# Kernel tuning notes

Measured on AMD Instinct MI355X. Metric: run time of the kernel, lower is better.

The kernel has to match this reference:

```python
import jax, jax.numpy as jnp
import numpy as np

N = 65536      # nodes in batched graph
E = 2097152    # edges (avg degree 32)
V = 1000       # chord vocabulary size
F_IN = 128     # chord feature dim
H = 256        # hidden_dim
OUT = 128      # out_dim
G = 256        # number of graphs in batch


def _gcn_layer(x, W, b, row, col, norm, n):
    # x: [n, f_in] -> [n, f_out]; PyG GCNConv: linear then normalized aggregation + bias
    x = x @ W
    msg = x[row] * norm[:, None]            # gather at source, scale by sym-norm
    return jax.ops.segment_sum(msg, col, num_segments=n) + b


def setup_inputs() -> dict:
    key = jax.random.key(0)
    ks = jax.random.split(key, 9)
    chord_feats = jax.random.normal(ks[0], (V, F_IN), jnp.float32)
    W1 = jax.random.normal(ks[1], (F_IN, H), jnp.float32) * 0.05
    b1 = jnp.zeros((H,), jnp.float32)
    W2 = jax.random.normal(ks[2], (H, OUT), jnp.float32) * 0.05
    b2 = jnp.zeros((OUT,), jnp.float32)
    edge_attr = jax.random.uniform(ks[3], (E,), jnp.float32)          # positive edge weights
    node_indices = jax.random.randint(ks[4], (N,), 0, V, jnp.int64)
    edge_index = jax.random.randint(ks[5], (2, E), 0, N, jnp.int64)
    batch_index = jnp.sort(jax.random.randint(ks[6], (N,), 0, G, jnp.int64))
    return {"chord_feats": chord_feats, "W1": W1, "b1": b1, "W2": W2, "b2": b2,
            "edge_attr": edge_attr, "node_indices": node_indices,
            "edge_index": edge_index, "batch_index": batch_index}


def reference(chord_feats, W1, b1, W2, b2, edge_attr, node_indices, edge_index, batch_index):
    loops = jnp.arange(N, dtype=edge_index.dtype)
    row = jnp.concatenate([edge_index[0], loops])   # source
    col = jnp.concatenate([edge_index[1], loops])   # target
    ew = jnp.concatenate([edge_attr, jnp.ones((N,), edge_attr.dtype)])  # self-loop weight 1
    # symmetric GCN normalization: D^-1/2 A D^-1/2
    deg = jax.ops.segment_sum(ew, col, num_segments=N)
    dis = jnp.where(deg > 0, jax.lax.rsqrt(jnp.maximum(deg, 1e-30)), 0.0)
    norm = dis[row] * ew * dis[col]

    x = chord_feats[node_indices]                   # [N, F_IN]
    x = jax.nn.relu(_gcn_layer(x, W1, b1, row, col, norm, N))
    x = jax.nn.relu(_gcn_layer(x, W2, b2, row, col, norm, N))

    # global_mean_pool over batch_index
    sums = jax.ops.segment_sum(x, batch_index, num_segments=G)
    counts = jax.ops.segment_sum(jnp.ones((N,), x.dtype), batch_index, num_segments=G)
    return sums / jnp.maximum(counts, 1.0)[:, None]
```

## Files before the change

### kernel.cpp

```cpp
#include <hip/hip_runtime.h>
#include <hip/hip_fp16.h>
#include <math.h>

constexpr int N_NODES = 65536;
constexpr int N_EDGES = 2097152;
constexpr int F_IN    = 128;
constexpr int H_DIM   = 256;
constexpr int O_DIM   = 128;
constexpr int N_GRAPH = 256;
constexpr int V_SIZE  = 1000;

constexpr int EPB  = 8192;
constexpr int NBLK = N_EDGES / EPB;
constexpr float FXP = 16777216.0f;


__global__ void k_init(float* __restrict__ pool, const int* __restrict__ batch,
                       float* __restrict__ cntf, const float* __restrict__ cf,
                       const float* __restrict__ W1, __half* __restrict__ cfW1) {
    __shared__ float xs[8 * F_IN];
    int i = blockIdx.x * blockDim.x + threadIdx.x;
    if (i < N_GRAPH * O_DIM) pool[i] = 0.0f;
    if (blockIdx.x == 0) {
        int g = threadIdx.x;
        int lo = 0, hi = N_NODES;
        while (lo < hi) { int m = (lo + hi) >> 1; if (batch[m] < g) lo = m + 1; else hi = m; }
        int start = lo;
        lo = 0; hi = N_NODES;
        while (lo < hi) { int m = (lo + hi) >> 1; if (batch[m] <= g) lo = m + 1; else hi = m; }
        cntf[g] = (float)(lo - start);
    }
    if (blockIdx.x < V_SIZE / 8) {
        int rb = blockIdx.x * 8;
        int t  = threadIdx.x;
        #pragma unroll
        for (int p = 0; p < 4; ++p) {
            int idx = p * 256 + t;
            int r = idx >> 7, k = idx & 127;
            xs[idx] = cf[(size_t)(rb + r) * F_IN + k];
        }
        __syncthreads();
        float acc[8] = {};
        for (int k = 0; k < F_IN; ++k) {
            float w = W1[k * H_DIM + t];
            #pragma unroll
            for (int j = 0; j < 8; ++j) acc[j] += xs[j * F_IN + k] * w;
        }
        #pragma unroll
        for (int j = 0; j < 8; ++j)
            cfW1[(size_t)(rb + j) * H_DIM + t] = __float2half(acc[j]);
    }
}


__global__ void k_hist(const int* __restrict__ col, int* __restrict__ hist) {
    __shared__ int h[256];
    int t = threadIdx.x;
    h[t] = 0;
    __syncthreads();
    int base = blockIdx.x * EPB;
    #pragma unroll
    for (int i = 0; i < EPB / 256; ++i)
        atomicAdd(&h[col[base + i * 256 + t] >> 8], 1);
    __syncthreads();
    hist[t * NBLK + blockIdx.x] = h[t];
}


__global__ void k_scan1(const int* __restrict__ in, int* __restrict__ out,
                        int* __restrict__ bsum) {
    __shared__ int s[256];
    int tid = threadIdx.x;
    int i = blockIdx.x * 256 + tid;
    int v = in[i];
    s[tid] = v;
    __syncthreads();
    for (int d = 1; d < 256; d <<= 1) {
        int t = (tid >= d) ? s[tid - d] : 0;
        __syncthreads();
        s[tid] += t;
        __syncthreads();
    }
    out[i] = s[tid] - v;
    if (tid == 255) bsum[blockIdx.x] = s[255];
}

__global__ void k_scan2(int* __restrict__ bsum) {
    __shared__ int s[256];
    int tid = threadIdx.x;
    int v = bsum[tid];
    s[tid] = v;
    __syncthreads();
    for (int d = 1; d < 256; d <<= 1) {
        int t = (tid >= d) ? s[tid - d] : 0;
        __syncthreads();
        s[tid] += t;
        __syncthreads();
    }
    bsum[tid] = s[tid] - v;
}


__global__ void k_part(const int* __restrict__ row, const int* __restrict__ col,
                       const float* __restrict__ ew, const int* __restrict__ nidx,
                       const int* __restrict__ hoffs, const int* __restrict__ bsum,
                       int2* __restrict__ part) {
    __shared__ int cur[256];
    int t = threadIdx.x;
    cur[t] = hoffs[t * NBLK + blockIdx.x] + bsum[t];
    __syncthreads();
    int base = blockIdx.x * EPB;
    for (int i = 0; i < EPB / 256; ++i) {
        int e = base + i * 256 + t;
        int r = row[e], c = col[e];
        unsigned hw = (unsigned)__half_as_ushort(__float2half(ew[e]));
        int vb = nidx[r];
        int slot = atomicAdd(&cur[c >> 8], 1);
        int2 rec;
        rec.x = (r << 16) | ((c & 255) << 8) | (vb >> 2);
        rec.y = (int)(((unsigned)(vb & 3) << 16) | hw);
        part[slot] = rec;
    }
}


__global__ void k_build1(const int* __restrict__ hoffs, const int* __restrict__ bsum,
                         const int2* __restrict__ part, float* __restrict__ dis,
                         int* __restrict__ offs) {
    __shared__ unsigned long long dc[256];
    __shared__ int sc[256];
    int t = threadIdx.x;
    int bucket = blockIdx.x;
    dc[t] = 0ULL;
    __syncthreads();
    int start = hoffs[bucket * NBLK] + bsum[bucket];
    int end   = (bucket == 255) ? N_EDGES : (hoffs[(bucket + 1) * NBLK] + bsum[bucket + 1]);
    for (int j = start + t; j < end; j += 256) {
        int2 rec = part[j];
        int dst = (rec.x >> 8) & 255;
        float w = __half2float(__ushort_as_half((unsigned short)(rec.y & 0xFFFF)));
        atomicAdd(&dc[dst], (1ULL << 40) |
                  (unsigned long long)(unsigned)(w * FXP + 0.5f));
    }
    __syncthreads();
    unsigned long long v = dc[t];
    float deg = 1.0f + (float)(v & 0xFFFFFFFFFFULL) * (1.0f / FXP);
    dis[bucket * 256 + t] = 1.0f / sqrtf(deg);
    int cnt = (int)(v >> 40);
    sc[t] = cnt;
    __syncthreads();
    for (int d = 1; d < 256; d <<= 1) {
        int x = (t >= d) ? sc[t - d] : 0;
        __syncthreads();
        sc[t] += x;
        __syncthreads();
    }
    offs[bucket * 256 + t] = start + sc[t] - cnt;
    if (bucket == 255 && t == 255) offs[N_NODES] = N_EDGES;
}


__global__ void k_build2(const int* __restrict__ hoffs, const int* __restrict__ bsum,
                         const int2* __restrict__ part, const float* __restrict__ dis,
                         const int* __restrict__ offs, int2* __restrict__ csr) {
    __shared__ int cur[256];
    int t = threadIdx.x;
    int bucket = blockIdx.x;
    cur[t] = offs[bucket * 256 + t];
    __syncthreads();
    int start = hoffs[bucket * NBLK] + bsum[bucket];
    int end   = (bucket == 255) ? N_EDGES : (hoffs[(bucket + 1) * NBLK] + bsum[bucket + 1]);
    for (int j = start + t; j < end; j += 256) {
        int2 rec = part[j];
        int dst = (rec.x >> 8) & 255;
        unsigned src = ((unsigned)rec.x) >> 16;
        int vb = ((rec.x & 255) << 2) | ((rec.y >> 16) & 3);
        float w = __half2float(__ushort_as_half((unsigned short)(rec.y & 0xFFFF)));
        float nm = dis[src] * w;
        int slot = atomicAdd(&cur[dst], 1);
        int2 e;
        e.x = (int)((src << 10) | (unsigned)vb);
        e.y = __float_as_int(nm);
        csr[slot] = e;
    }
}


__global__ void k_agg1(const int2* __restrict__ cfW1, const int* __restrict__ nidx,
                       const float* __restrict__ dis, const int* __restrict__ offs,
                       const int2* __restrict__ csr, const float4* __restrict__ b1f4,
                       int2* __restrict__ h1) {
    int wave = threadIdx.x >> 6;
    int lane = threadIdx.x & 63;
    int c = blockIdx.x * 4 + wave;
    float d = dis[c];
    int2 sp = cfW1[(size_t)nidx[c] * 64 + lane];
    float2 sa = __half22float2(*(__half2*)&sp.x);
    float2 sb = __half22float2(*(__half2*)&sp.y);
    float4 esum = {0.f, 0.f, 0.f, 0.f};
    int a0 = offs[c], a1 = offs[c + 1];
    int s = a0;
    for (; s + 8 <= a1; s += 8) {
        int sb_i = __builtin_amdgcn_readfirstlane(s);
        int2 e[8];
        #pragma unroll
        for (int u = 0; u < 8; ++u) e[u] = csr[sb_i + u];
        int2 v[8];
        #pragma unroll
        for (int u = 0; u < 8; ++u)
            v[u] = cfW1[(size_t)(e[u].x & 1023) * 64 + lane];
        #pragma unroll
        for (int u = 0; u < 8; ++u) {
            float n = __int_as_float(e[u].y);
            float2 va = __half22float2(*(__half2*)&v[u].x);
            float2 vb = __half22float2(*(__half2*)&v[u].y);
            esum.x += va.x * n; esum.y += va.y * n;
            esum.z += vb.x * n; esum.w += vb.y * n;
        }
    }
    for (; s < a1; ++s) {
        int sb_i = __builtin_amdgcn_readfirstlane(s);
        int2 e0 = csr[sb_i];
        int2 v0 = cfW1[(size_t)(e0.x & 1023) * 64 + lane];
        float n = __int_as_float(e0.y);
        float2 va = __half22float2(*(__half2*)&v0.x);
        float2 vb = __half22float2(*(__half2*)&v0.y);
        esum.x += va.x * n; esum.y += va.y * n;
        esum.z += vb.x * n; esum.w += vb.y * n;
    }
    float4 bb = b1f4[lane];
    float dd = d * d;
    float r0 = bb.x + sa.x * dd + d * esum.x;
    float r1 = bb.y + sa.y * dd + d * esum.y;
    float r2 = bb.z + sb.x * dd + d * esum.z;
    float r3 = bb.w + sb.y * dd + d * esum.w;
    r0 = r0 > 0.f ? r0 : 0.f;  r1 = r1 > 0.f ? r1 : 0.f;
    r2 = r2 > 0.f ? r2 : 0.f;  r3 = r3 > 0.f ? r3 : 0.f;
    float2 p0 = {r0, r1}, p1 = {r2, r3};
    __half2 ha = __float22half2_rn(p0);
    __half2 hb = __float22half2_rn(p1);
    int2 outv;
    outv.x = *(int*)&ha;
    outv.y = *(int*)&hb;
    h1[(size_t)c * 64 + lane] = outv;
}


__global__ void k_gemm2(const __half* __restrict__ h1, const float* __restrict__ W2,
                        __half* __restrict__ xw2h) {
    __shared__ float xs[32 * H_DIM];
    int nb = blockIdx.x * 32;
    int t  = threadIdx.x;
    const int4* src = (const int4*)(h1 + (size_t)nb * H_DIM);
    float4* dst4 = (float4*)xs;
    #pragma unroll
    for (int p = 0; p < 4; ++p) {
        int4 pk = src[p * 256 + t];
        __half2 ha = *(__half2*)&pk.x, hb = *(__half2*)&pk.y;
        __half2 hc = *(__half2*)&pk.z, hd = *(__half2*)&pk.w;
        float2 fa = __half22float2(ha), fb = __half22float2(hb);
        float2 fc = __half22float2(hc), fd = __half22float2(hd);
        float4 A; A.x = fa.x; A.y = fa.y; A.z = fb.x; A.w = fb.y;
        float4 B; B.x = fc.x; B.y = fc.y; B.z = fd.x; B.w = fd.y;
        dst4[(p * 256 + t) * 2]     = A;
        dst4[(p * 256 + t) * 2 + 1] = B;
    }
    __syncthreads();
    int o  = t & 63;
    int jg = t >> 6;
    const float* xsj = xs + jg * 8 * H_DIM;
    float acc[8][2] = {};
    for (int k = 0; k < H_DIM; ++k) {
        float w0 = W2[k * O_DIM + o];
        float w1 = W2[k * O_DIM + o + 64];
        #pragma unroll
        for (int j = 0; j < 8; ++j) {
            float x = xsj[j * H_DIM + k];
            acc[j][0] += x * w0; acc[j][1] += x * w1;
        }
    }
    #pragma unroll
    for (int j = 0; j < 8; ++j) {
        size_t base = (size_t)(nb + jg * 8 + j) * O_DIM + o;
        xw2h[base]      = __float2half(acc[j][0]);
        xw2h[base + 64] = __float2half(acc[j][1]);
    }
}


__global__ void k_agg2_pool(const __half2* __restrict__ xw2h, const float* __restrict__ b2,
                            const float* __restrict__ dis, const int* __restrict__ offs,
                            const int2* __restrict__ csr, const int* __restrict__ batch,
                            float* __restrict__ pool) {
    __shared__ float2 red[4][64];
    __shared__ int bgs[4];
    int wave = threadIdx.x >> 6;
    int lane = threadIdx.x & 63;
    int c = blockIdx.x * 4 + wave;
    float d = dis[c];
    float2 self = __half22float2(xw2h[(size_t)c * 64 + lane]);
    float2 bb = ((const float2*)b2)[lane];
    float2 esum = {0.f, 0.f};
    int s0 = offs[c], s1 = offs[c + 1];
    int s = s0;
    for (; s + 8 <= s1; s += 8) {
        int sb_i = __builtin_amdgcn_readfirstlane(s);
        int2 e[8];
        #pragma unroll
        for (int u = 0; u < 8; ++u) e[u] = csr[sb_i + u];
        float2 v[8];
        #pragma unroll
        for (int u = 0; u < 8; ++u)
            v[u] = __half22float2(xw2h[(size_t)(e[u].x >> 10) * 64 + lane]);
        #pragma unroll
        for (int u = 0; u < 8; ++u) {
            float n = __int_as_float(e[u].y);
            esum.x += v[u].x * n; esum.y += v[u].y * n;
        }
    }
    for (; s < s1; ++s) {
        int sb_i = __builtin_amdgcn_readfirstlane(s);
        int2 e0 = csr[sb_i];
        float2 v0 = __half22float2(xw2h[(size_t)(e0.x >> 10) * 64 + lane]);
        float n0 = __int_as_float(e0.y);
        esum.x += v0.x * n0; esum.y += v0.y * n0;
    }
    float dd = d * d;
    float2 acc;
    acc.x = bb.x + self.x * dd + d * esum.x;
    acc.y = bb.y + self.y * dd + d * esum.y;
    acc.x = acc.x > 0.0f ? acc.x : 0.0f;
    acc.y = acc.y > 0.0f ? acc.y : 0.0f;
    red[wave][lane] = acc;
    if (lane == 0) bgs[wave] = batch[c];
    __syncthreads();
    if (wave == 0) {
        float2 a = red[0][lane];
        int cg = bgs[0];
        #pragma unroll
        for (int w = 1; w < 4; ++w) {
            int g = bgs[w];
            float2 r = red[w][lane];
            if (g == cg) { a.x += r.x; a.y += r.y; }
            else {
                atomicAdd(&pool[cg * O_DIM + 2 * lane], a.x);
                atomicAdd(&pool[cg * O_DIM + 2 * lane + 1], a.y);
                a = r; cg = g;
            }
        }
        atomicAdd(&pool[cg * O_DIM + 2 * lane], a.x);
        atomicAdd(&pool[cg * O_DIM + 2 * lane + 1], a.y);
    }
}

__global__ void k_final(const float* __restrict__ pool, const float* __restrict__ cnt,
                        float* __restrict__ out) {
    int t = blockIdx.x * blockDim.x + threadIdx.x;
    if (t < N_GRAPH * O_DIM) {
        int g = t / O_DIM;
        out[t] = pool[t] / fmaxf(cnt[g], 1.0f);
    }
}


extern "C" void kernel_launch(void* const* d_in, const int* in_sizes, int n_in,
                              void* d_out, int out_size, void* d_ws, size_t ws_size,
                              hipStream_t stream) {
    const float* cf   = (const float*)d_in[0];
    const float* W1   = (const float*)d_in[1];
    const float* b1   = (const float*)d_in[2];
    const float* W2   = (const float*)d_in[3];
    const float* b2   = (const float*)d_in[4];
    const float* ew   = (const float*)d_in[5];
    const int*   nidx = (const int*)d_in[6];
    const int*   eidx = (const int*)d_in[7];
    const int*   bidx = (const int*)d_in[8];
    float* out = (float*)d_out;

    const int* row = eidx;
    const int* col = eidx + N_EDGES;

    char* ws = (char*)d_ws;
    size_t off = 0;
    int*   hist  = (int*)  (ws + off); off += (size_t)N_NODES * 4;
    int*   hoffs = (int*)  (ws + off); off += (size_t)N_NODES * 4;
    int*   bsum  = (int*)  (ws + off); off += 4096;
    float* dis   = (float*)(ws + off); off += (size_t)N_NODES * 4;
    int*   offs  = (int*)  (ws + off); off += (size_t)(N_NODES + 16) * 4;
    int2*  csr   = (int2*) (ws + off); off += (size_t)N_EDGES * 8;
    float* pool  = (float*)(ws + off); off += (size_t)(N_GRAPH * O_DIM + N_GRAPH) * 4;
    __half* cfW1 = (__half*)(ws + off); off += (size_t)V_SIZE * H_DIM * 2;
    off = (off + 255) & ~(size_t)255;
    int2*  part  = (int2*) (ws + off); off += (size_t)N_EDGES * 8;
    __half* h1   = (__half*)(ws + off);
    __half* xw2h = (__half*)part;
    float* cntf  = pool + N_GRAPH * O_DIM;

    k_init<<<N_GRAPH * O_DIM / 256, 256, 0, stream>>>(pool, bidx, cntf, cf, W1, cfW1);
    k_hist<<<NBLK, 256, 0, stream>>>(col, hist);
    k_scan1<<<256, 256, 0, stream>>>(hist, hoffs, bsum);
    k_scan2<<<1, 256, 0, stream>>>(bsum);

    k_part<<<NBLK, 256, 0, stream>>>(row, col, ew, nidx, hoffs, bsum, part);
    k_build1<<<256, 256, 0, stream>>>(hoffs, bsum, part, dis, offs);
    k_build2<<<256, 256, 0, stream>>>(hoffs, bsum, part, dis, offs, csr);

    k_agg1<<<N_NODES / 4, 256, 0, stream>>>((const int2*)cfW1, nidx, dis, offs, csr,
                                            (const float4*)b1, (int2*)h1);

    k_gemm2<<<N_NODES / 32, 256, 0, stream>>>(h1, W2, xw2h);
    k_agg2_pool<<<N_NODES / 4, 256, 0, stream>>>((const __half2*)xw2h, b2, dis, offs, csr,
                                                 bidx, pool);

    k_final<<<(N_GRAPH * O_DIM + 255) / 256, 256, 0, stream>>>(pool, cntf, out);
}
```

Measured before the change: 366.8 us.

## Use fp16 MFMA matrix cores for the second-layer GEMM with a pretransposed W2

Replaces the scalar FP32 shared-memory GEMM for h1·W2 with a wave-level MFMA 16x16x32 f16 kernel. Each wave loads its A rows straight into registers and streams B tiles from an fp16, transposed copy of W2. That W2T copy is built by extra blocks added to the init kernel. The goal is to remove the FMA-bound scalar loop and the fp16-to-fp32 shared-memory staging, at the cost of fp16 weight precision and uncoalesced 2-byte output stores.

```diff
diff --git a/kernel.cpp b/kernel.cpp
--- a/kernel.cpp
+++ b/kernel.cpp
@@ -14,10 +14,14 @@
 constexpr int NBLK = N_EDGES / EPB;
 constexpr float FXP = 16777216.0f;
 
+typedef _Float16 half8 __attribute__((ext_vector_type(8)));
+typedef float floatx4 __attribute__((ext_vector_type(4)));
+
 
 __global__ void k_init(float* __restrict__ pool, const int* __restrict__ batch,
                        float* __restrict__ cntf, const float* __restrict__ cf,
-                       const float* __restrict__ W1, __half* __restrict__ cfW1) {
+                       const float* __restrict__ W1, __half* __restrict__ cfW1,
+                       const float* __restrict__ W2, _Float16* __restrict__ W2T) {
     __shared__ float xs[8 * F_IN];
     int i = blockIdx.x * blockDim.x + threadIdx.x;
     if (i < N_GRAPH * O_DIM) pool[i] = 0.0f;
@@ -49,6 +53,11 @@
         #pragma unroll
         for (int j = 0; j < 8; ++j)
             cfW1[(size_t)(rb + j) * H_DIM + t] = __float2half(acc[j]);
+    }
+    if (blockIdx.x >= 128) {
+        int idx = (blockIdx.x - 128) * 256 + threadIdx.x;
+        int nn = idx >> 8, kk = idx & 255;
+        W2T[idx] = (_Float16)W2[kk * O_DIM + nn];
     }
 }
 
@@ -246,44 +255,32 @@
 }
 
 
-__global__ void k_gemm2(const __half* __restrict__ h1, const float* __restrict__ W2,
+__global__ void k_gemm2(const _Float16* __restrict__ h1, const _Float16* __restrict__ W2T,
                         __half* __restrict__ xw2h) {
-    __shared__ float xs[32 * H_DIM];
-    int nb = blockIdx.x * 32;
-    int t  = threadIdx.x;
-    const int4* src = (const int4*)(h1 + (size_t)nb * H_DIM);
-    float4* dst4 = (float4*)xs;
+    int wave = threadIdx.x >> 6;
+    int lane = threadIdx.x & 63;
+    int quad = lane >> 4;
+    int n    = lane & 15;
+    int tm   = blockIdx.x * 4 + wave;
+    const _Float16* arow = h1 + (size_t)(tm * 16 + n) * H_DIM;
+    half8 a[8];
     #pragma unroll
-    for (int p = 0; p < 4; ++p) {
-        int4 pk = src[p * 256 + t];
-        __half2 ha = *(__half2*)&pk.x, hb = *(__half2*)&pk.y;
-        __half2 hc = *(__half2*)&pk.z, hd = *(__half2*)&pk.w;
-        float2 fa = __half22float2(ha), fb = __half22float2(hb);
-        float2 fc = __half22float2(hc), fd = __half22float2(hd);
-        float4 A; A.x = fa.x; A.y = fa.y; A.z = fb.x; A.w = fb.y;
-        float4 B; B.x = fc.x; B.y = fc.y; B.z = fd.x; B.w = fd.y;
-        dst4[(p * 256 + t) * 2]     = A;
-        dst4[(p * 256 + t) * 2 + 1] = B;
-    }
-    __syncthreads();
-    int o  = t & 63;
-    int jg = t >> 6;
-    const float* xsj = xs + jg * 8 * H_DIM;
-    float acc[8][2] = {};
-    for (int k = 0; k < H_DIM; ++k) {
-        float w0 = W2[k * O_DIM + o];
-        float w1 = W2[k * O_DIM + o + 64];
-        #pragma unroll
-        for (int j = 0; j < 8; ++j) {
-            float x = xsj[j * H_DIM + k];
-            acc[j][0] += x * w0; acc[j][1] += x * w1;
-        }
-    }
+    for (int kt = 0; kt < 8; ++kt)
+        a[kt] = *(const half8*)(arow + kt * 32 + quad * 8);
     #pragma unroll
-    for (int j = 0; j < 8; ++j) {
-        size_t base = (size_t)(nb + jg * 8 + j) * O_DIM + o;
-        xw2h[base]      = __float2half(acc[j][0]);
-        xw2h[base + 64] = __float2half(acc[j][1]);
+    for (int nt = 0; nt < 8; ++nt) {
+        floatx4 acc = {0.f, 0.f, 0.f, 0.f};
+        const _Float16* brow = W2T + (size_t)(nt * 16 + n) * H_DIM;
+        #pragma unroll
+        for (int kt = 0; kt < 8; ++kt) {
+            half8 b = *(const half8*)(brow + kt * 32 + quad * 8);
+            acc = __builtin_amdgcn_mfma_f32_16x16x32_f16(a[kt], b, acc, 0, 0, 0);
+        }
+        #pragma unroll
+        for (int r = 0; r < 4; ++r) {
+            int rowi = tm * 16 + quad * 4 + r;
+            xw2h[(size_t)rowi * O_DIM + nt * 16 + n] = __float2half(acc[r]);
+        }
     }
 }
 
@@ -390,13 +387,14 @@
     int2*  csr   = (int2*) (ws + off); off += (size_t)N_EDGES * 8;
     float* pool  = (float*)(ws + off); off += (size_t)(N_GRAPH * O_DIM + N_GRAPH) * 4;
     __half* cfW1 = (__half*)(ws + off); off += (size_t)V_SIZE * H_DIM * 2;
+    _Float16* W2T = (_Float16*)(ws + off); off += (size_t)O_DIM * H_DIM * 2;
     off = (off + 255) & ~(size_t)255;
     int2*  part  = (int2*) (ws + off); off += (size_t)N_EDGES * 8;
     __half* h1   = (__half*)(ws + off);
     __half* xw2h = (__half*)part;
     float* cntf  = pool + N_GRAPH * O_DIM;
 
-    k_init<<<N_GRAPH * O_DIM / 256, 256, 0, stream>>>(pool, bidx, cntf, cf, W1, cfW1);
+    k_init<<<256, 256, 0, stream>>>(pool, bidx, cntf, cf, W1, cfW1, W2, W2T);
     k_hist<<<NBLK, 256, 0, stream>>>(col, hist);
     k_scan1<<<256, 256, 0, stream>>>(hist, hoffs, bsum);
     k_scan2<<<1, 256, 0, stream>>>(bsum);
@@ -408,7 +406,7 @@
     k_agg1<<<N_NODES / 4, 256, 0, stream>>>((const int2*)cfW1, nidx, dis, offs, csr,
                                             (const float4*)b1, (int2*)h1);
 
-    k_gemm2<<<N_NODES / 32, 256, 0, stream>>>(h1, W2, xw2h);
+    k_gemm2<<<N_NODES / 64, 256, 0, stream>>>((const _Float16*)h1, W2T, xw2h);
     k_agg2_pool<<<N_NODES / 4, 256, 0, stream>>>((const __half2*)xw2h, b2, dis, offs, csr,
                                                  bidx, pool);
 
```

Result: faster. 346.8 us, median of 2 (-5.4%).
